# Performance work log

Hardware: AMD Instinct MI355X
Metric: run time of the kernel (lower is better)

The kernel has to match this reference:

```python
import jax, jax.numpy as jnp
import numpy as np
import math

B, S, D, L, H, V, MAXP = 8, 512, 1024, 6, 8, 32000, 4096
HD = D // H
FF = 4 * D
EPS = 1e-5
SCALE = 1.0 / math.sqrt(HD)


def _ln(x, g, b):
    m = x.mean(-1, keepdims=True)
    xm = x - m
    v = (xm * xm).mean(-1, keepdims=True)
    return xm * jax.lax.rsqrt(v + EPS) * g + b


def setup_inputs() -> dict:
    key = jax.random.key(0)
    ks = jax.random.split(key, 16)
    std = 0.02
    inp = {
        'input_ids': jax.random.randint(ks[0], (B, S), 0, V, dtype=jnp.int32),
        'attention_mask': jnp.ones((B, S), dtype=jnp.int32),
        'current_position': 0,
        'tok_emb': jax.random.normal(ks[1], (V, D), jnp.float32) * std,
        'pos_emb': jax.random.normal(ks[2], (MAXP, D), jnp.float32) * std,
        'ln1_s': jnp.ones((L, D), jnp.float32),
        'ln1_b': jnp.zeros((L, D), jnp.float32),
        'Wq': jax.random.normal(ks[3], (L, D, D), jnp.float32) * std,
        'bq': jnp.zeros((L, D), jnp.float32),
        'Wk': jax.random.normal(ks[4], (L, D, D), jnp.float32) * std,
        'bk': jnp.zeros((L, D), jnp.float32),
        'Wv': jax.random.normal(ks[5], (L, D, D), jnp.float32) * std,
        'bv': jnp.zeros((L, D), jnp.float32),
        'Wo': jax.random.normal(ks[6], (L, D, D), jnp.float32) * std,
        'bo': jnp.zeros((L, D), jnp.float32),
        'ln2_s': jnp.ones((L, D), jnp.float32),
        'ln2_b': jnp.zeros((L, D), jnp.float32),
        'W1': jax.random.normal(ks[7], (L, D, FF), jnp.float32) * std,
        'b1': jnp.zeros((L, FF), jnp.float32),
        'W2': jax.random.normal(ks[8], (L, FF, D), jnp.float32) * std,
        'b2': jnp.zeros((L, D), jnp.float32),
        'lnf_s': jnp.ones((D,), jnp.float32),
        'lnf_b': jnp.zeros((D,), jnp.float32),
        'Wout': jax.random.normal(ks[9], (D, D), jnp.float32) * std,
        'bout': jnp.zeros((D,), jnp.float32),
    }
    return inp


def reference(input_ids, attention_mask, current_position, tok_emb, pos_emb,
              ln1_s, ln1_b, Wq, bq, Wk, bk, Wv, bv, Wo, bo,
              ln2_s, ln2_b, W1, b1, W2, b2, lnf_s, lnf_b, Wout, bout):
    pos = current_position + jnp.arange(S)  # [S]
    h = tok_emb[input_ids] + pos_emb[pos][None, :, :]  # [B,S,D]
    pad = (attention_mask == 0)[:, None, None, :]  # [B,1,1,S] key-padding mask

    def layer(h, p):
        (l1s, l1b, wq, bq_, wk, bk_, wv, bv_, wo, bo_,
         l2s, l2b, w1, b1_, w2, b2_) = p
        x = _ln(h, l1s, l1b)
        q = (x @ wq + bq_).reshape(B, S, H, HD).transpose(0, 2, 1, 3)
        k = (x @ wk + bk_).reshape(B, S, H, HD).transpose(0, 2, 1, 3)
        v = (x @ wv + bv_).reshape(B, S, H, HD).transpose(0, 2, 1, 3)
        scores = jnp.einsum('bhqd,bhkd->bhqk', q, k) * SCALE
        scores = jnp.where(pad, -10000.0, scores)
        attn = jax.nn.softmax(scores, axis=-1)
        o = jnp.einsum('bhqk,bhkd->bhqd', attn, v)
        o = o.transpose(0, 2, 1, 3).reshape(B, S, D)
        h = h + (o @ wo + bo_)
        x = _ln(h, l2s, l2b)
        mlp = jax.nn.gelu(x @ w1 + b1_, approximate=False) @ w2 + b2_
        return h + mlp, None

    h, _ = jax.lax.scan(layer, h, (ln1_s, ln1_b, Wq, bq, Wk, bk, Wv, bv, Wo, bo,
                                   ln2_s, ln2_b, W1, b1, W2, b2))
    h = _ln(h, lnf_s, lnf_b)
    return h @ Wout + bout
```

## Files before the change

kernel.cpp:

```cpp
#include <hip/hip_runtime.h>
#include <hip/hip_bf16.h>
#include <math.h>

#define BB 8
#define SS 512
#define DD 1024
#define LL 6
#define HH 8
#define HDD 128
#define FFF 4096
#define EPSF 1e-5f
#define SCALEF 0.08838834764831845f

typedef __attribute__((ext_vector_type(8))) _Float16 f16x8;
typedef __attribute__((ext_vector_type(4))) _Float16 f16x4;
typedef __attribute__((ext_vector_type(4))) float f32x4;

__device__ __forceinline__ void gload16(const void* g, void* l) {
  __builtin_amdgcn_global_load_lds(
      (const __attribute__((address_space(1))) void*)g,
      (__attribute__((address_space(3))) void*)l, 16, 0, 0);
}

__global__ __launch_bounds__(256, 3) void gemmk_kernel(
    const _Float16* __restrict__ Ag, const _Float16* __restrict__ Bg,
    const float* __restrict__ bias, void* __restrict__ outp,
    const int* __restrict__ amask, int Ndim, int Kdim, int Kstr,
    long zsA, long zsB, long zsOut, int emode) {
  __shared__ _Float16 lA[4096];
  __shared__ _Float16 lB[4096];
  const int tid = threadIdx.x;
  const int lane = tid & 63;
  const int wid = tid >> 6;
  const int z = blockIdx.z;
  const int m0 = blockIdx.y * 128;
  const int n0 = blockIdx.x * 128;
  const long K2 = (long)Kstr * 2;
  const _Float16* Az = Ag + (long)z * zsA + (long)m0 * Kstr;
  const _Float16* Bz = Bg + (long)z * zsB + (long)n0 * Kstr;

  const int wm = (wid >> 1) * 64;
  const int wn = (wid & 1) * 64;
  const int r16 = lane & 15;
  const int kq = lane >> 4;

  const char* As[2];
  const char* Bs[2];
  int ld[2];
#pragma unroll
  for (int i = 0; i < 2; ++i) {
    const int r = wid * 32 + i * 16 + (lane >> 2);
    const int sc = ((lane & 3) << 4) ^ (((r >> 1) & 3) << 4);
    As[i] = (const char*)Az + (long)r * K2 + sc;
    Bs[i] = (const char*)Bz + (long)r * K2 + sc;
    ld[i] = (wid * 128 + i * 64 + lane) * 16;
  }
  int adA[4], adB[4];
#pragma unroll
  for (int mi = 0; mi < 4; ++mi) {
    const int R = wm + mi * 16 + r16;
    adA[mi] = R * 64 + ((kq ^ ((R >> 1) & 3)) << 4);
  }
#pragma unroll
  for (int ni = 0; ni < 4; ++ni) {
    const int R = wn + ni * 16 + r16;
    adB[ni] = R * 64 + ((kq ^ ((R >> 1) & 3)) << 4);
  }

  f32x4 acc[4][4];
#pragma unroll
  for (int mi = 0; mi < 4; ++mi)
#pragma unroll
    for (int ni = 0; ni < 4; ++ni) acc[mi][ni] = (f32x4){0.f, 0.f, 0.f, 0.f};

  const int nt = Kdim >> 5;
  for (int t = 0; t < nt; ++t) {
    const int kb = t << 6;
    __syncthreads();
#pragma unroll
    for (int i = 0; i < 2; ++i) {
      gload16(As[i] + kb, (char*)lA + ld[i]);
      gload16(Bs[i] + kb, (char*)lB + ld[i]);
    }
    __syncthreads();
    f16x8 af[4], bf[4];
#pragma unroll
    for (int mi = 0; mi < 4; ++mi)
      af[mi] = *(const f16x8*)((const char*)lA + adA[mi]);
#pragma unroll
    for (int ni = 0; ni < 4; ++ni)
      bf[ni] = *(const f16x8*)((const char*)lB + adB[ni]);
#pragma unroll
    for (int mi = 0; mi < 4; ++mi)
#pragma unroll
      for (int ni = 0; ni < 4; ++ni)
        acc[mi][ni] = __builtin_amdgcn_mfma_f32_16x16x32_f16(
            af[mi], bf[ni], acc[mi][ni], 0, 0, 0);
  }

  _Float16* outH = (_Float16*)outp + (long)z * zsOut;
  const int rj = (lane >> 4) << 2;
  const long MSZq = (long)BB * SS * DD;
#pragma unroll
  for (int mi = 0; mi < 4; ++mi) {
#pragma unroll
    for (int ni = 0; ni < 4; ++ni) {
      const int col = n0 + wn + ni * 16 + r16;
#pragma unroll
      for (int j = 0; j < 4; ++j) {
        const int row = m0 + wm + mi * 16 + rj + j;
        float vv = acc[mi][ni][j];
        if (emode == 1) {
          vv += bias[col];
          int wsel = col >> 10, c = col & 1023;
          int b_ = row >> 9, s_ = row & 511;
          int hh = c >> 7, hd_ = c & 127;
          if (wsel < 2) {
            outH[wsel * MSZq + (((long)(b_ * HH + hh)) * SS + s_) * HDD + hd_] =
                (_Float16)vv;
          } else {
            outH[2 * MSZq + (((long)(b_ * HH + hh)) * HDD + hd_) * SS + s_] =
                (_Float16)vv;
          }
        } else if (emode == 2) {
          int b_ = z >> 3;
          vv = (amask[b_ * SS + col] == 0) ? -10000.0f : vv * SCALEF;
          outH[(long)row * Ndim + col] = (_Float16)vv;
        } else if (emode == 3) {
          int b_ = z >> 3, hh = z & 7;
          outH[((long)(b_ * SS + row)) * DD + hh * HDD + col] = (_Float16)vv;
        } else if (emode == 5) {
          vv += bias[col];
          vv = 0.5f * vv * (1.0f + erff(vv * 0.70710678118654752f));
          outH[(long)row * Ndim + col] = (_Float16)vv;
        } else {
          outH[(long)row * Ndim + col] = (_Float16)vv;
        }
      }
    }
  }
}

__global__ __launch_bounds__(256) void reduce_ln_kernel(
    const _Float16* __restrict__ parts, int npart,
    const float* __restrict__ res, const float* __restrict__ bias,
    const float* __restrict__ lg, const float* __restrict__ lb,
    float* __restrict__ hout, _Float16* __restrict__ xout, long pzs) {
  const int row = blockIdx.x;
  const int c = threadIdx.x << 2;
  const long base = (long)row * DD + c;
  float4 a = *reinterpret_cast<const float4*>(&bias[c]);
  if (res) {
    const float4 r = *reinterpret_cast<const float4*>(&res[base]);
    a.x += r.x; a.y += r.y; a.z += r.z; a.w += r.w;
  }
  for (int p = 0; p < npart; ++p) {
    const f16x4 hpv = *reinterpret_cast<const f16x4*>(&parts[p * pzs + base]);
    a.x += (float)hpv[0]; a.y += (float)hpv[1];
    a.z += (float)hpv[2]; a.w += (float)hpv[3];
  }
  *reinterpret_cast<float4*>(&hout[base]) = a;
  if (!lg) return;
  float s = a.x + a.y + a.z + a.w;
  float ss = a.x * a.x + a.y * a.y + a.z * a.z + a.w * a.w;
#pragma unroll
  for (int off = 32; off; off >>= 1) {
    s += __shfl_down(s, off);
    ss += __shfl_down(ss, off);
  }
  __shared__ float red[8];
  const int wid = threadIdx.x >> 6, lane = threadIdx.x & 63;
  if (lane == 0) { red[wid] = s; red[4 + wid] = ss; }
  __syncthreads();
  if (threadIdx.x == 0) {
    s = red[0] + red[1] + red[2] + red[3];
    ss = red[4] + red[5] + red[6] + red[7];
    float mean = s * (1.0f / DD);
    float var = ss * (1.0f / DD) - mean * mean;
    red[0] = mean;
    red[1] = rsqrtf(var + EPSF);
  }
  __syncthreads();
  const float mean = red[0], rstd = red[1];
  const float4 gv = *reinterpret_cast<const float4*>(&lg[c]);
  const float4 bv = *reinterpret_cast<const float4*>(&lb[c]);
  f16x4 o;
  o[0] = (_Float16)((a.x - mean) * rstd * gv.x + bv.x);
  o[1] = (_Float16)((a.y - mean) * rstd * gv.y + bv.y);
  o[2] = (_Float16)((a.z - mean) * rstd * gv.z + bv.z);
  o[3] = (_Float16)((a.w - mean) * rstd * gv.w + bv.w);
  *reinterpret_cast<f16x4*>(&xout[base]) = o;
}

__global__ __launch_bounds__(256) void embed_ln_kernel(
    const int* __restrict__ ids, const int* __restrict__ curpos,
    const float* __restrict__ tok, const float* __restrict__ pos,
    const float* __restrict__ lg, const float* __restrict__ lb,
    float* __restrict__ h, _Float16* __restrict__ x) {
  const int rs = blockIdx.x;
  const int s_ = rs & (SS - 1);
  const int t = ids[rs];
  const int p = curpos[0] + s_;
  const int c = threadIdx.x << 2;
  const float4 tv = *reinterpret_cast<const float4*>(&tok[(long)t * DD + c]);
  const float4 pv = *reinterpret_cast<const float4*>(&pos[(long)p * DD + c]);
  float4 a = {tv.x + pv.x, tv.y + pv.y, tv.z + pv.z, tv.w + pv.w};
  *reinterpret_cast<float4*>(&h[(long)rs * DD + c]) = a;
  float s = a.x + a.y + a.z + a.w;
  float ss = a.x * a.x + a.y * a.y + a.z * a.z + a.w * a.w;
#pragma unroll
  for (int off = 32; off; off >>= 1) {
    s += __shfl_down(s, off);
    ss += __shfl_down(ss, off);
  }
  __shared__ float red[8];
  const int wid = threadIdx.x >> 6, lane = threadIdx.x & 63;
  if (lane == 0) { red[wid] = s; red[4 + wid] = ss; }
  __syncthreads();
  if (threadIdx.x == 0) {
    s = red[0] + red[1] + red[2] + red[3];
    ss = red[4] + red[5] + red[6] + red[7];
    float mean = s * (1.0f / DD);
    float var = ss * (1.0f / DD) - mean * mean;
    red[0] = mean;
    red[1] = rsqrtf(var + EPSF);
  }
  __syncthreads();
  const float mean = red[0], rstd = red[1];
  const float4 gv = *reinterpret_cast<const float4*>(&lg[c]);
  const float4 bv = *reinterpret_cast<const float4*>(&lb[c]);
  f16x4 o;
  o[0] = (_Float16)((a.x - mean) * rstd * gv.x + bv.x);
  o[1] = (_Float16)((a.y - mean) * rstd * gv.y + bv.y);
  o[2] = (_Float16)((a.z - mean) * rstd * gv.z + bv.z);
  o[3] = (_Float16)((a.w - mean) * rstd * gv.w + bv.w);
  *reinterpret_cast<f16x4*>(&x[(long)rs * DD + c]) = o;
}

__global__ __launch_bounds__(256) void softmax_kernel(_Float16* __restrict__ p) {
  const long row = (long)blockIdx.x * 4 + (threadIdx.x >> 6);
  const int lane = threadIdx.x & 63;
  _Float16* pr = p + row * SS;
  f16x8 hv = *reinterpret_cast<const f16x8*>(&pr[lane * 8]);
  float v[8];
#pragma unroll
  for (int j = 0; j < 8; ++j) v[j] = (float)hv[j];
  float m = v[0];
#pragma unroll
  for (int j = 1; j < 8; ++j) m = fmaxf(m, v[j]);
#pragma unroll
  for (int off = 1; off < 64; off <<= 1) m = fmaxf(m, __shfl_xor(m, off));
  float sum = 0.f;
#pragma unroll
  for (int j = 0; j < 8; ++j) {
    v[j] = expf(v[j] - m);
    sum += v[j];
  }
#pragma unroll
  for (int off = 1; off < 64; off <<= 1) sum += __shfl_xor(sum, off);
  const float inv = 1.0f / sum;
#pragma unroll
  for (int j = 0; j < 8; ++j) hv[j] = (_Float16)(v[j] * inv);
  *reinterpret_cast<f16x8*>(&pr[lane * 8]) = hv;
}

__global__ __launch_bounds__(256) void wtrans_kernel(
    const float* __restrict__ W, _Float16* __restrict__ WT, int K, int N) {
  __shared__ float t[64][65];
  const int n0 = blockIdx.x * 64, k0 = blockIdx.y * 64;
  const int tx = threadIdx.x & 63;
  const int ty = threadIdx.x >> 6;
#pragma unroll
  for (int i = 0; i < 16; ++i)
    t[i * 4 + ty][tx] = W[(long)(k0 + i * 4 + ty) * N + n0 + tx];
  __syncthreads();
#pragma unroll
  for (int i = 0; i < 16; ++i) {
    const int r = i * 4 + ty;
    WT[(long)(n0 + r) * K + k0 + tx] = (_Float16)t[tx][r];
  }
}

__global__ __launch_bounds__(256) void packb_kernel(
    const float* __restrict__ bq, const float* __restrict__ bk,
    const float* __restrict__ bv, float* __restrict__ bqkv) {
  const int i = blockIdx.x * 256 + threadIdx.x;
  const int l = i / (3 * DD), j = i % (3 * DD);
  float v;
  if (j < DD) v = bq[l * DD + j];
  else if (j < 2 * DD) v = bk[l * DD + j - DD];
  else v = bv[l * DD + j - 2 * DD];
  bqkv[i] = v;
}

extern "C" void kernel_launch(void* const* d_in, const int* in_sizes, int n_in,
                              void* d_out, int out_size, void* d_ws,
                              size_t ws_size, hipStream_t stream) {
  const int* ids = (const int*)d_in[0];
  const int* amask = (const int*)d_in[1];
  const int* curp = (const int*)d_in[2];
  const float* tok = (const float*)d_in[3];
  const float* pose = (const float*)d_in[4];
  const float* ln1s = (const float*)d_in[5];
  const float* ln1b = (const float*)d_in[6];
  const float* Wq = (const float*)d_in[7];
  const float* bq = (const float*)d_in[8];
  const float* Wk = (const float*)d_in[9];
  const float* bk = (const float*)d_in[10];
  const float* Wv = (const float*)d_in[11];
  const float* bv = (const float*)d_in[12];
  const float* Wo = (const float*)d_in[13];
  const float* bo = (const float*)d_in[14];
  const float* ln2s = (const float*)d_in[15];
  const float* ln2b = (const float*)d_in[16];
  const float* W1 = (const float*)d_in[17];
  const float* b1 = (const float*)d_in[18];
  const float* W2 = (const float*)d_in[19];
  const float* b2 = (const float*)d_in[20];
  const float* lnfs = (const float*)d_in[21];
  const float* lnfb = (const float*)d_in[22];
  const float* Wout = (const float*)d_in[23];
  const float* bout = (const float*)d_in[24];

  const long MSZ = (long)BB * SS * DD;
  char* wsp = (char*)d_ws;
  float* h = (float*)wsp;
  _Float16* x = (_Float16*)(wsp + 16u * 1024 * 1024);
  _Float16* q = x + MSZ;
  _Float16* kb = q + MSZ;
  _Float16* vt = kb + MSZ;
  _Float16* big = vt + MSZ;
  _Float16* wqkvT = big + (long)BB * HH * SS * SS;
  _Float16* woT = wqkvT + 3L * DD * DD;
  _Float16* w1T = woT + (long)DD * DD;
  _Float16* w2T = w1T + (long)DD * FFF;
  float* bqkv = (float*)(w2T + (long)FFF * DD);
  _Float16* parts = (_Float16*)(bqkv + LL * 3 * DD);

  const int M = BB * SS;
  dim3 blk(256);
  const long pzs = (long)M * DD;

  embed_ln_kernel<<<M, blk, 0, stream>>>(ids, curp, tok, pose, ln1s, ln1b, h, x);
  packb_kernel<<<(LL * 3 * DD) / 256, blk, 0, stream>>>(bq, bk, bv, bqkv);

  const dim3 gQKV(3 * DD / 128, M / 128, 1);
  const dim3 gS(SS / 128, SS / 128, BB * HH);
  const dim3 gV(1, SS / 128, BB * HH);
  const dim3 gF1(FFF / 128, M / 128, 1);
  const dim3 gK2(DD / 128, M / 128, 2);
  const dim3 gK4(DD / 128, M / 128, 4);
  const dim3 gWt(DD / 64, DD / 64);
  const dim3 gW1t(FFF / 64, DD / 64);
  const dim3 gW2t(DD / 64, FFF / 64);

  for (int l = 0; l < LL; ++l) {
    wtrans_kernel<<<gWt, blk, 0, stream>>>(Wq + (long)l * DD * DD, wqkvT, DD, DD);
    wtrans_kernel<<<gWt, blk, 0, stream>>>(Wk + (long)l * DD * DD,
                                           wqkvT + (long)DD * DD, DD, DD);
    wtrans_kernel<<<gWt, blk, 0, stream>>>(Wv + (long)l * DD * DD,
                                           wqkvT + 2L * DD * DD, DD, DD);
    wtrans_kernel<<<gWt, blk, 0, stream>>>(Wo + (long)l * DD * DD, woT, DD, DD);
    wtrans_kernel<<<gW1t, blk, 0, stream>>>(W1 + (long)l * DD * FFF, w1T, DD, FFF);
    wtrans_kernel<<<gW2t, blk, 0, stream>>>(W2 + (long)l * FFF * DD, w2T, FFF, DD);

    gemmk_kernel<<<gQKV, blk, 0, stream>>>(x, wqkvT, bqkv + l * 3 * DD, q,
                                           nullptr, 3 * DD, DD, DD, 0, 0, 0, 1);
    gemmk_kernel<<<gS, blk, 0, stream>>>(q, kb, nullptr, big, amask, SS, HDD,
                                         HDD, (long)SS * HDD, (long)SS * HDD,
                                         (long)SS * SS, 2);
    softmax_kernel<<<(BB * HH * SS) / 4, blk, 0, stream>>>(big);
    gemmk_kernel<<<gV, blk, 0, stream>>>(big, vt, nullptr, x, nullptr, HDD, SS,
                                         SS, (long)SS * SS, (long)SS * HDD, 0,
                                         3);
    gemmk_kernel<<<gK2, blk, 0, stream>>>(x, woT, nullptr, parts, nullptr, DD,
                                          DD / 2, DD, DD / 2, DD / 2, pzs, 6);
    reduce_ln_kernel<<<M, blk, 0, stream>>>(parts, 2, h, bo + l * DD,
                                            ln2s + l * DD, ln2b + l * DD, h, x,
                                            pzs);
    gemmk_kernel<<<gF1, blk, 0, stream>>>(x, w1T, b1 + l * FFF, big, nullptr,
                                          FFF, DD, DD, 0, 0, 0, 5);
    gemmk_kernel<<<gK4, blk, 0, stream>>>(big, w2T, nullptr, parts, nullptr,
                                          DD, FFF / 4, FFF, FFF / 4, FFF / 4,
                                          pzs, 6);
    const float* ng = (l < LL - 1) ? (ln1s + (l + 1) * DD) : lnfs;
    const float* nb = (l < LL - 1) ? (ln1b + (l + 1) * DD) : lnfb;
    reduce_ln_kernel<<<M, blk, 0, stream>>>(parts, 4, h, b2 + l * DD, ng, nb,
                                            h, x, pzs);
  }
  wtrans_kernel<<<gWt, blk, 0, stream>>>(Wout, woT, DD, DD);
  gemmk_kernel<<<gK2, blk, 0, stream>>>(x, woT, nullptr, parts, nullptr, DD,
                                        DD / 2, DD, DD / 2, DD / 2, pzs, 6);
  reduce_ln_kernel<<<M, blk, 0, stream>>>(parts, 2, nullptr, bout, nullptr,
                                          nullptr, (float*)d_out, nullptr, pzs);
}
```

Measured before the change: 1.879 ms.

## Fuse softmax into PV GEMM, double GEMM K-tile, batch QKV/O weight transposes

Three changes land together. The separate softmax pass is replaced by a kernel that reads raw scores, applies an online softmax per row block and multiplies by V straight from global memory, which removes a full read-modify-write of the score matrix. The shared GEMM kernel now stages a 64-wide K tile (double the LDS) with an 8-way XOR swizzle, halving the number of barrier pairs. The four per-layer D×D weight transposes are merged into one launch. The risks are that the fused kernel has no LDS staging for S and V, so its global loads may be poorly reused, and that the larger LDS footprint may lower GEMM occupancy.

```diff
diff --git a/kernel.cpp b/kernel.cpp
--- a/kernel.cpp
+++ b/kernel.cpp
@@ -27,8 +27,8 @@
     const float* __restrict__ bias, void* __restrict__ outp,
     const int* __restrict__ amask, int Ndim, int Kdim, int Kstr,
     long zsA, long zsB, long zsOut, int emode) {
-  __shared__ _Float16 lA[4096];
-  __shared__ _Float16 lB[4096];
+  __shared__ _Float16 lA[8192];
+  __shared__ _Float16 lB[8192];
   const int tid = threadIdx.x;
   const int lane = tid & 63;
   const int wid = tid >> 6;
@@ -44,27 +44,28 @@
   const int r16 = lane & 15;
   const int kq = lane >> 4;
 
-  const char* As[2];
-  const char* Bs[2];
-  int ld[2];
-#pragma unroll
-  for (int i = 0; i < 2; ++i) {
-    const int r = wid * 32 + i * 16 + (lane >> 2);
-    const int sc = ((lane & 3) << 4) ^ (((r >> 1) & 3) << 4);
+  const char* As[4];
+  const char* Bs[4];
+  int ldd[4];
+#pragma unroll
+  for (int i = 0; i < 4; ++i) {
+    const int idx = tid + i * 256;
+    const int r = idx >> 3;
+    const int sc = ((idx & 7) << 4) ^ ((r & 7) << 4);
     As[i] = (const char*)Az + (long)r * K2 + sc;
     Bs[i] = (const char*)Bz + (long)r * K2 + sc;
-    ld[i] = (wid * 128 + i * 64 + lane) * 16;
+    ldd[i] = idx * 16;
   }
   int adA[4], adB[4];
 #pragma unroll
   for (int mi = 0; mi < 4; ++mi) {
     const int R = wm + mi * 16 + r16;
-    adA[mi] = R * 64 + ((kq ^ ((R >> 1) & 3)) << 4);
+    adA[mi] = R * 128 + ((kq * 16) ^ ((R & 7) << 4));
   }
 #pragma unroll
   for (int ni = 0; ni < 4; ++ni) {
     const int R = wn + ni * 16 + r16;
-    adB[ni] = R * 64 + ((kq ^ ((R >> 1) & 3)) << 4);
+    adB[ni] = R * 128 + ((kq * 16) ^ ((R & 7) << 4));
   }
 
   f32x4 acc[4][4];
@@ -73,29 +74,38 @@
 #pragma unroll
     for (int ni = 0; ni < 4; ++ni) acc[mi][ni] = (f32x4){0.f, 0.f, 0.f, 0.f};
 
-  const int nt = Kdim >> 5;
+  const int nt = Kdim >> 6;
   for (int t = 0; t < nt; ++t) {
-    const int kb = t << 6;
+    const int kb = t << 7;
     __syncthreads();
 #pragma unroll
-    for (int i = 0; i < 2; ++i) {
-      gload16(As[i] + kb, (char*)lA + ld[i]);
-      gload16(Bs[i] + kb, (char*)lB + ld[i]);
+    for (int i = 0; i < 4; ++i) {
+      gload16(As[i] + kb, (char*)lA + ldd[i]);
+      gload16(Bs[i] + kb, (char*)lB + ldd[i]);
     }
     __syncthreads();
-    f16x8 af[4], bf[4];
-#pragma unroll
-    for (int mi = 0; mi < 4; ++mi)
-      af[mi] = *(const f16x8*)((const char*)lA + adA[mi]);
-#pragma unroll
-    for (int ni = 0; ni < 4; ++ni)
-      bf[ni] = *(const f16x8*)((const char*)lB + adB[ni]);
-#pragma unroll
-    for (int mi = 0; mi < 4; ++mi)
-#pragma unroll
-      for (int ni = 0; ni < 4; ++ni)
-        acc[mi][ni] = __builtin_amdgcn_mfma_f32_16x16x32_f16(
-            af[mi], bf[ni], acc[mi][ni], 0, 0, 0);
+#pragma unroll
+    for (int kk = 0; kk < 2; ++kk) {
+      f16x8 af[4], bf[4];
+#pragma unroll
+      for (int mi = 0; mi < 4; ++mi) {
+        const int R = wm + mi * 16 + r16;
+        af[mi] = *(const f16x8*)((const char*)lA + R * 128 +
+                                 ((kk * 64 + kq * 16) ^ ((R & 7) << 4)));
+      }
+#pragma unroll
+      for (int ni = 0; ni < 4; ++ni) {
+        const int R = wn + ni * 16 + r16;
+        bf[ni] = *(const f16x8*)((const char*)lB + R * 128 +
+                                 ((kk * 64 + kq * 16) ^ ((R & 7) << 4)));
+      }
+#pragma unroll
+      for (int mi = 0; mi < 4; ++mi)
+#pragma unroll
+        for (int ni = 0; ni < 4; ++ni)
+          acc[mi][ni] = __builtin_amdgcn_mfma_f32_16x16x32_f16(
+              af[mi], bf[ni], acc[mi][ni], 0, 0, 0);
+    }
   }
 
   _Float16* outH = (_Float16*)outp + (long)z * zsOut;
@@ -126,9 +136,6 @@
           int b_ = z >> 3;
           vv = (amask[b_ * SS + col] == 0) ? -10000.0f : vv * SCALEF;
           outH[(long)row * Ndim + col] = (_Float16)vv;
-        } else if (emode == 3) {
-          int b_ = z >> 3, hh = z & 7;
-          outH[((long)(b_ * SS + row)) * DD + hh * HDD + col] = (_Float16)vv;
         } else if (emode == 5) {
           vv += bias[col];
           vv = 0.5f * vv * (1.0f + erff(vv * 0.70710678118654752f));
@@ -139,6 +146,114 @@
       }
     }
   }
+}
+
+__global__ __launch_bounds__(256) void flashpv_kernel(
+    const _Float16* __restrict__ Sg, const _Float16* __restrict__ Vt,
+    _Float16* __restrict__ xout) {
+  const int tid = threadIdx.x;
+  const int lane = tid & 63;
+  const int wid = tid >> 6;
+  const int bh = blockIdx.y;
+  const int q0 = blockIdx.x * 128;
+  const int wm = (wid >> 1) * 64;
+  const int wn = (wid & 1) * 64;
+  const int r16 = lane & 15;
+  const int kq = lane >> 4;
+  const int rj = kq << 2;
+  const _Float16* Sb = Sg + (long)bh * SS * SS + (long)q0 * SS;
+  const _Float16* Vb = Vt + (long)bh * HDD * SS;
+
+  f32x4 acc[4][4];
+#pragma unroll
+  for (int mi = 0; mi < 4; ++mi)
+#pragma unroll
+    for (int ni = 0; ni < 4; ++ni) acc[mi][ni] = (f32x4){0.f, 0.f, 0.f, 0.f};
+  float m[4], l[4];
+#pragma unroll
+  for (int mi = 0; mi < 4; ++mi) {
+    m[mi] = -INFINITY;
+    l[mi] = 0.f;
+  }
+
+  for (int kt = 0; kt < 4; ++kt) {
+    const int kvb = kt * 128;
+    f16x8 pa[4][4];
+    float rf[4];
+#pragma unroll
+    for (int mi = 0; mi < 4; ++mi) {
+      f16x8 sf[4];
+#pragma unroll
+      for (int ks = 0; ks < 4; ++ks)
+        sf[ks] = *(const f16x8*)(Sb + (long)(wm + mi * 16 + r16) * SS + kvb +
+                                 ks * 32 + kq * 8);
+      float tm = -INFINITY;
+#pragma unroll
+      for (int ks = 0; ks < 4; ++ks)
+#pragma unroll
+        for (int e = 0; e < 8; ++e) tm = fmaxf(tm, (float)sf[ks][e]);
+      tm = fmaxf(tm, __shfl_xor(tm, 16));
+      tm = fmaxf(tm, __shfl_xor(tm, 32));
+      const float mn = fmaxf(m[mi], tm);
+      rf[mi] = __expf(m[mi] - mn);
+      m[mi] = mn;
+      float rs = 0.f;
+#pragma unroll
+      for (int ks = 0; ks < 4; ++ks) {
+        f16x8 p;
+#pragma unroll
+        for (int e = 0; e < 8; ++e) {
+          const float pv = __expf((float)sf[ks][e] - mn);
+          rs += pv;
+          p[e] = (_Float16)pv;
+        }
+        pa[mi][ks] = p;
+      }
+      rs += __shfl_xor(rs, 16);
+      rs += __shfl_xor(rs, 32);
+      l[mi] = l[mi] * rf[mi] + rs;
+    }
+#pragma unroll
+    for (int mi = 0; mi < 4; ++mi)
+#pragma unroll
+      for (int j = 0; j < 4; ++j) {
+        const float f = __shfl(rf[mi], (lane & 48) | (rj + j));
+#pragma unroll
+        for (int ni = 0; ni < 4; ++ni) acc[mi][ni][j] *= f;
+      }
+#pragma unroll
+    for (int ks = 0; ks < 4; ++ks) {
+      f16x8 bf[4];
+#pragma unroll
+      for (int ni = 0; ni < 4; ++ni)
+        bf[ni] = *(const f16x8*)(Vb + (long)(wn + ni * 16 + r16) * SS + kvb +
+                                 ks * 32 + kq * 8);
+#pragma unroll
+      for (int mi = 0; mi < 4; ++mi)
+#pragma unroll
+        for (int ni = 0; ni < 4; ++ni)
+          acc[mi][ni] = __builtin_amdgcn_mfma_f32_16x16x32_f16(
+              pa[mi][ks], bf[ni], acc[mi][ni], 0, 0, 0);
+    }
+  }
+
+  float linv[4];
+#pragma unroll
+  for (int mi = 0; mi < 4; ++mi) linv[mi] = 1.0f / l[mi];
+  const int b_ = bh >> 3, hh = bh & 7;
+#pragma unroll
+  for (int mi = 0; mi < 4; ++mi)
+#pragma unroll
+    for (int j = 0; j < 4; ++j) {
+      const float f = __shfl(linv[mi], (lane & 48) | (rj + j));
+      const int row = q0 + wm + mi * 16 + rj + j;
+#pragma unroll
+      for (int ni = 0; ni < 4; ++ni) {
+        const int col = wn + ni * 16 + r16;
+        xout[((long)(b_ * SS + row)) * DD + hh * HDD + col] =
+            (_Float16)(acc[mi][ni][j] * f);
+      }
+    }
 }
 
 __global__ __launch_bounds__(256) void reduce_ln_kernel(
@@ -237,31 +352,26 @@
   *reinterpret_cast<f16x4*>(&x[(long)rs * DD + c]) = o;
 }
 
-__global__ __launch_bounds__(256) void softmax_kernel(_Float16* __restrict__ p) {
-  const long row = (long)blockIdx.x * 4 + (threadIdx.x >> 6);
-  const int lane = threadIdx.x & 63;
-  _Float16* pr = p + row * SS;
-  f16x8 hv = *reinterpret_cast<const f16x8*>(&pr[lane * 8]);
-  float v[8];
-#pragma unroll
-  for (int j = 0; j < 8; ++j) v[j] = (float)hv[j];
-  float m = v[0];
-#pragma unroll
-  for (int j = 1; j < 8; ++j) m = fmaxf(m, v[j]);
-#pragma unroll
-  for (int off = 1; off < 64; off <<= 1) m = fmaxf(m, __shfl_xor(m, off));
-  float sum = 0.f;
-#pragma unroll
-  for (int j = 0; j < 8; ++j) {
-    v[j] = expf(v[j] - m);
-    sum += v[j];
-  }
-#pragma unroll
-  for (int off = 1; off < 64; off <<= 1) sum += __shfl_xor(sum, off);
-  const float inv = 1.0f / sum;
-#pragma unroll
-  for (int j = 0; j < 8; ++j) hv[j] = (_Float16)(v[j] * inv);
-  *reinterpret_cast<f16x8*>(&pr[lane * 8]) = hv;
+__global__ __launch_bounds__(256) void wtrans4_kernel(
+    const float* __restrict__ Wq, const float* __restrict__ Wk,
+    const float* __restrict__ Wv, const float* __restrict__ Wo,
+    _Float16* __restrict__ qkvT, _Float16* __restrict__ woT) {
+  __shared__ float t[64][65];
+  const int zz = blockIdx.z;
+  const float* W = (zz == 0) ? Wq : (zz == 1) ? Wk : (zz == 2) ? Wv : Wo;
+  _Float16* WT = (zz < 3) ? (qkvT + (long)zz * DD * DD) : woT;
+  const int n0 = blockIdx.x * 64, k0 = blockIdx.y * 64;
+  const int tx = threadIdx.x & 63;
+  const int ty = threadIdx.x >> 6;
+#pragma unroll
+  for (int i = 0; i < 16; ++i)
+    t[i * 4 + ty][tx] = W[(long)(k0 + i * 4 + ty) * DD + n0 + tx];
+  __syncthreads();
+#pragma unroll
+  for (int i = 0; i < 16; ++i) {
+    const int r = i * 4 + ty;
+    WT[(long)(n0 + r) * DD + k0 + tx] = (_Float16)t[tx][r];
+  }
 }
 
 __global__ __launch_bounds__(256) void wtrans_kernel(
@@ -346,21 +456,19 @@
 
   const dim3 gQKV(3 * DD / 128, M / 128, 1);
   const dim3 gS(SS / 128, SS / 128, BB * HH);
-  const dim3 gV(1, SS / 128, BB * HH);
+  const dim3 gPV(SS / 128, BB * HH);
   const dim3 gF1(FFF / 128, M / 128, 1);
   const dim3 gK2(DD / 128, M / 128, 2);
   const dim3 gK4(DD / 128, M / 128, 4);
+  const dim3 gWt4(DD / 64, DD / 64, 4);
   const dim3 gWt(DD / 64, DD / 64);
   const dim3 gW1t(FFF / 64, DD / 64);
   const dim3 gW2t(DD / 64, FFF / 64);
 
   for (int l = 0; l < LL; ++l) {
-    wtrans_kernel<<<gWt, blk, 0, stream>>>(Wq + (long)l * DD * DD, wqkvT, DD, DD);
-    wtrans_kernel<<<gWt, blk, 0, stream>>>(Wk + (long)l * DD * DD,
-                                           wqkvT + (long)DD * DD, DD, DD);
-    wtrans_kernel<<<gWt, blk, 0, stream>>>(Wv + (long)l * DD * DD,
-                                           wqkvT + 2L * DD * DD, DD, DD);
-    wtrans_kernel<<<gWt, blk, 0, stream>>>(Wo + (long)l * DD * DD, woT, DD, DD);
+    const long lo = (long)l * DD * DD;
+    wtrans4_kernel<<<gWt4, blk, 0, stream>>>(Wq + lo, Wk + lo, Wv + lo, Wo + lo,
+                                             wqkvT, woT);
     wtrans_kernel<<<gW1t, blk, 0, stream>>>(W1 + (long)l * DD * FFF, w1T, DD, FFF);
     wtrans_kernel<<<gW2t, blk, 0, stream>>>(W2 + (long)l * FFF * DD, w2T, FFF, DD);
 
@@ -369,10 +477,7 @@
     gemmk_kernel<<<gS, blk, 0, stream>>>(q, kb, nullptr, big, amask, SS, HDD,
                                          HDD, (long)SS * HDD, (long)SS * HDD,
                                          (long)SS * SS, 2);
-    softmax_kernel<<<(BB * HH * SS) / 4, blk, 0, stream>>>(big);
-    gemmk_kernel<<<gV, blk, 0, stream>>>(big, vt, nullptr, x, nullptr, HDD, SS,
-                                         SS, (long)SS * SS, (long)SS * HDD, 0,
-                                         3);
+    flashpv_kernel<<<gPV, blk, 0, stream>>>(big, vt, x);
     gemmk_kernel<<<gK2, blk, 0, stream>>>(x, woT, nullptr, parts, nullptr, DD,
                                           DD / 2, DD, DD / 2, DD / 2, pzs, 6);
     reduce_ln_kernel<<<M, blk, 0, stream>>>(parts, 2, h, bo + l * DD,
```

After: 1.638 ms. 12.8% less time.
